# Kernel optimization log

Measured on AMD Instinct MI355X. Metric: run time of the kernel, lower is better.

Reference implementation:

```python
import jax, jax.numpy as jnp
import numpy as np

B = 4096      # number of trees
DEPTH = 7     # complete binary tree depth -> N = 2**DEPTH - 1 = 127 nodes (heap order)
I_DIM = 300
H_DIM = 150


def setup_inputs() -> dict:
    key = jax.random.key(0)
    ks = jax.random.split(key, 6)
    N = 2 ** DEPTH - 1
    x = jax.random.normal(ks[0], (B, N, I_DIM), dtype=jnp.float32)
    Wiuo = jax.random.normal(ks[1], (3 * H_DIM, I_DIM), dtype=jnp.float32) / np.sqrt(I_DIM)
    Uiuo = jax.random.normal(ks[2], (3 * H_DIM, H_DIM), dtype=jnp.float32) / np.sqrt(H_DIM)
    biuo = jax.random.normal(ks[3], (1, 3 * H_DIM), dtype=jnp.float32) * 0.02
    Uf_w = jax.random.normal(ks[4], (H_DIM, H_DIM), dtype=jnp.float32) / np.sqrt(H_DIM)
    Uf_b = jax.random.normal(ks[5], (H_DIM,), dtype=jnp.float32) * 0.02
    return {"x": x, "Wiuo": Wiuo, "Uiuo": Uiuo, "biuo": biuo, "Uf_w": Uf_w, "Uf_b": Uf_b}


def reference(x, Wiuo, Uiuo, biuo, Uf_w, Uf_b):
    # Child-sum Tree-LSTM on complete binary trees (heap ordering).
    # Level d occupies node indices [2^d - 1, 2^(d+1) - 1); leaves at d = DEPTH-1.
    Bsz, N, _ = x.shape
    H = Uf_w.shape[0]
    # Input projection for all nodes (dropout in eval mode = identity)
    iuo_x = jnp.einsum('bni,ki->bnk', x, Wiuo)  # [B, N, 3H]
    h = jnp.zeros((Bsz, N, H), x.dtype)
    c = jnp.zeros((Bsz, N, H), x.dtype)
    for d in reversed(range(DEPTH)):  # leaves -> root (static loop over tree levels)
        start = 2 ** d - 1
        size = 2 ** d
        iuo = iuo_x[:, start:start + size]  # [B, size, 3H]
        if d == DEPTH - 1:
            c_sum = jnp.zeros((Bsz, size, H), x.dtype)
        else:
            cstart = 2 ** (d + 1) - 1
            ch = h[:, cstart:cstart + 2 * size].reshape(Bsz, size, 2, H)
            cc = c[:, cstart:cstart + 2 * size].reshape(Bsz, size, 2, H)
            h_tilda = ch.sum(axis=2)  # sum of children hidden states
            f = jax.nn.sigmoid(jnp.einsum('bskh,gh->bskg', ch, Uf_w) + Uf_b)
            c_sum = (f * cc).sum(axis=2)
            iuo = iuo + jnp.einsum('bsh,kh->bsk', h_tilda, Uiuo)
        iuo = iuo + biuo
        i_g, u_g, o_g = jnp.split(iuo, 3, axis=-1)
        c_new = jax.nn.sigmoid(i_g) * jnp.tanh(u_g) + c_sum
        h_new = jax.nn.sigmoid(o_g) * jnp.tanh(c_new)
        h = h.at[:, start:start + size].set(h_new)
        c = c.at[:, start:start + size].set(c_new)
    return h
```

## Files before the change

kernel.cpp:

```cpp
#include <hip/hip_runtime.h>

typedef float  f32x4  __attribute__((ext_vector_type(4)));
typedef short  s16x8  __attribute__((ext_vector_type(8)));
typedef short  s16x4  __attribute__((ext_vector_type(4)));
typedef __bf16 bf16x8 __attribute__((ext_vector_type(8)));

namespace {
constexpr int BATCH = 4096, DEPTH_ = 7, NN = 127, CN = 126, IDIM = 300, HD = 150;
constexpr int NW = 10, NT = 640;
constexpr int XSTR = 328;
constexpr int CSTR = 164;
constexpr int BCS  = 40;

constexpr int WSLAB = 19456;
constexpr int FSLAB = 6656;
constexpr int WCH = 38, FCH = 13;
constexpr int W_SH = 10 * WSLAB, U_SH = 5 * WSLAB, F_SH = 5 * FSLAB;
constexpr size_t C_FLOATS = (size_t)BATCH * CN * HD;

constexpr int LEAF_XS = 128 * XSTR;
constexpr int INT_CHS = 128 * CSTR;
constexpr int INT_XS  = 64 * XSTR;
constexpr int LDS_LEAF_B = (LEAF_XS + 2 * WSLAB) * 2;
constexpr int LDS_INT_B  = (INT_CHS + INT_XS + 2 * WSLAB) * 2;

__device__ __forceinline__ short f2bf(float f) {
    union { __bf16 b; short s; } u; u.b = (__bf16)f; return u.s;
}
__device__ __forceinline__ float bf2f(short s) {
    union { float f; unsigned u; } v; v.u = ((unsigned)(unsigned short)s) << 16; return v.f;
}
__device__ __forceinline__ float sig_(float x)  { return 1.0f / (1.0f + __expf(-x)); }
__device__ __forceinline__ float tanh_(float x) { float e = __expf(2.0f * x); return 1.0f - 2.0f / (e + 1.0f); }

__device__ __forceinline__ f32x4 MFMA(s16x8 a, s16x8 b, f32x4 c) {
    return __builtin_amdgcn_mfma_f32_16x16x32_bf16(a, b, c, 0, 0, 0);
}

typedef const __attribute__((address_space(1))) unsigned int* gp_t;
typedef __attribute__((address_space(3))) unsigned int* lp_t;
__device__ __forceinline__ void stage_slab(const short* g, short* l, int nch, int wv, int ln) {
    const char* gb = (const char*)g;
    char* lb = (char*)l;
    for (int c = wv; c < nch; c += NW)
        __builtin_amdgcn_global_load_lds((gp_t)(gb + c * 1024 + ln * 16),
                                         (lp_t)(lb + c * 1024 + ln * 16), 16, 0, 0);
}
}

__global__ __launch_bounds__(256)
void prep_w(const float* __restrict__ Wiuo, const float* __restrict__ Uiuo,
            const float* __restrict__ Ufw, short* __restrict__ dst) {
    int i = blockIdx.x * 256 + threadIdx.x;
    short v = 0;
    if (i < W_SH) {
        int kb = i / WSLAB, r = i - kb * WSLAB;
        if (r < 480 * BCS) {
            int cs = r / BCS, j = r - cs * BCS;
            int g = cs / 160, cp = cs - g * 160, k = kb * 32 + j;
            if (cp < HD && j < 32 && k < IDIM) v = f2bf(Wiuo[(size_t)(g*HD + cp)*IDIM + k]);
        }
        dst[i] = v;
    } else if (i < W_SH + U_SH) {
        int q = i - W_SH;
        int kb = q / WSLAB, r = q - kb * WSLAB;
        if (r < 480 * BCS) {
            int cs = r / BCS, j = r - cs * BCS;
            int g = cs / 160, cp = cs - g * 160, k = kb * 32 + j;
            if (cp < HD && j < 32 && k < HD) v = f2bf(Uiuo[(size_t)(g*HD + cp)*HD + k]);
        }
        dst[i] = v;
    } else if (i < W_SH + U_SH + F_SH) {
        int q = i - W_SH - U_SH;
        int kb = q / FSLAB, r = q - kb * FSLAB;
        if (r < 160 * BCS) {
            int cs = r / BCS, j = r - cs * BCS, k = kb * 32 + j;
            if (cs < HD && j < 32 && k < HD) v = f2bf(Ufw[(size_t)cs*HD + k]);
        }
        dst[i] = v;
    }
}

template<bool INTERNAL>
__global__ __launch_bounds__(NT)
void lvl_kernel(const float* __restrict__ x,
                const short* __restrict__ Wsl, const short* __restrict__ Usl,
                const short* __restrict__ Fsl,
                const float* __restrict__ biuo, const float* __restrict__ Ufb,
                float* __restrict__ h_all, float* __restrict__ c_all,
                int start, int lg, int cstart)
{
    constexpr int MT = INTERNAL ? 4 : 8;
    constexpr int BM = 16 * MT;
    extern __shared__ short smem[];
    short* chs = smem;
    short* xs  = INTERNAL ? (smem + INT_CHS) : smem;
    short* fg  = xs;
    short* B0  = INTERNAL ? (smem + INT_CHS + INT_XS) : (smem + LEAF_XS);
    short* B1  = B0 + WSLAB;

    const int t    = threadIdx.x;
    const int wv   = t >> 6;
    const int ln   = t & 63;
    const int l15  = ln & 15;
    const int kg   = ln >> 4;
    const int row0 = blockIdx.x * BM;
    const int size = 1 << lg;
    const int c16  = 16 * wv;

    stage_slab(Wsl, B0, WCH, wv, ln);
    {
        constexpr int NQ = XSTR / 4;
        for (int q = t; q < BM * NQ; q += NT) {
            int lr = q / NQ, i0 = (q - lr * NQ) * 4;
            int row = row0 + lr, b = row >> lg, s = row & (size - 1);
            s16x4 v = {0,0,0,0};
            if (i0 < IDIM) {
                const float4 f = *(const float4*)(x + ((size_t)b*NN + start + s)*IDIM + i0);
                v = s16x4{ f2bf(f.x), f2bf(f.y), f2bf(f.z), f2bf(f.w) };
            }
            *(s16x4*)&xs[lr * XSTR + i0] = v;
        }
    }
    if (INTERNAL) {
        constexpr int NQ = CSTR / 4;
        for (int q = t; q < 2 * BM * NQ; q += NT) {
            int cl = q / NQ, i0 = (q - cl * NQ) * 4;
            int lr = cl >> 1, cc = cl & 1;
            int row = row0 + lr, b = row >> lg, s = row & (size - 1);
            const float* hp = h_all + ((size_t)b*NN + cstart + 2*s + cc) * HD;
            s16x4 v = {0,0,0,0};
            if (i0 + 3 < HD) {
                float2 f0 = *(const float2*)(hp + i0);
                float2 f1 = *(const float2*)(hp + i0 + 2);
                v = s16x4{ f2bf(f0.x), f2bf(f0.y), f2bf(f1.x), f2bf(f1.y) };
            } else if (i0 < HD) {
                float2 f0 = *(const float2*)(hp + i0);
                v = s16x4{ f2bf(f0.x), f2bf(f0.y), 0, 0 };
            }
            *(s16x4*)&chs[cl * CSTR + i0] = v;
        }
    }
    __syncthreads();

    f32x4 acc[MT][3] = {};

    #pragma unroll
    for (int kb = 0; kb < 10; ++kb) {
        short* bcur = (kb & 1) ? B1 : B0;
        short* bnxt = (kb & 1) ? B0 : B1;
        if (kb < 9)            stage_slab(Wsl + (kb+1)*WSLAB, bnxt, WCH, wv, ln);
        else if (INTERNAL)     stage_slab(Usl, bnxt, WCH, wv, ln);
        s16x8 a[MT];
        #pragma unroll
        for (int mt = 0; mt < MT; ++mt)
            a[mt] = *(const s16x8*)&xs[(16*mt + l15) * XSTR + kb*32 + kg*8];
        #pragma unroll
        for (int g = 0; g < 3; ++g) {
            s16x8 bf = *(const s16x8*)&bcur[(g*160 + c16 + l15) * BCS + kg*8];
            #pragma unroll
            for (int mt = 0; mt < MT; ++mt)
                acc[mt][g] = MFMA(a[mt], bf, acc[mt][g]);
        }
        __syncthreads();
    }

    f32x4 facc[2*MT] = {};

    if (INTERNAL) {
        #pragma unroll
        for (int ku = 0; ku < 5; ++ku) {
            int s = 10 + ku;
            short* bcur = (s & 1) ? B1 : B0;
            short* bnxt = (s & 1) ? B0 : B1;
            if (ku < 4) stage_slab(Usl + (ku+1)*WSLAB, bnxt, WCH, wv, ln);
            else        stage_slab(Fsl, bnxt, FCH, wv, ln);
            int ka = ku*32 + kg*8;
            s16x8 hs[MT];
            #pragma unroll
            for (int mt = 0; mt < MT; ++mt) {
                int pr = 16*mt + l15;
                s16x8 h0 = *(const s16x8*)&chs[(2*pr    ) * CSTR + ka];
                s16x8 h1 = *(const s16x8*)&chs[(2*pr + 1) * CSTR + ka];
                union { bf16x8 b; s16x8 s; } u0, u1, uo;
                u0.s = h0; u1.s = h1;
                #pragma unroll
                for (int e = 0; e < 8; ++e)
                    uo.b[e] = (__bf16)((float)u0.b[e] + (float)u1.b[e]);
                hs[mt] = uo.s;
            }
            #pragma unroll
            for (int g = 0; g < 3; ++g) {
                s16x8 bf = *(const s16x8*)&bcur[(g*160 + c16 + l15) * BCS + kg*8];
                #pragma unroll
                for (int mt = 0; mt < MT; ++mt)
                    acc[mt][g] = MFMA(hs[mt], bf, acc[mt][g]);
            }
            __syncthreads();
        }

        #pragma unroll
        for (int kf = 0; kf < 5; ++kf) {
            int s = 15 + kf;
            short* bcur = (s & 1) ? B1 : B0;
            short* bnxt = (s & 1) ? B0 : B1;
            if (kf < 4) stage_slab(Fsl + (kf+1)*FSLAB, bnxt, FCH, wv, ln);
            int ka = kf*32 + kg*8;
            s16x8 bf = *(const s16x8*)&bcur[(c16 + l15) * BCS + kg*8];
            #pragma unroll
            for (int rt = 0; rt < 2*MT; ++rt) {
                s16x8 af = *(const s16x8*)&chs[(16*rt + l15) * CSTR + ka];
                facc[rt] = MFMA(af, bf, facc[rt]);
            }
            __syncthreads();
        }

        {
            int c = c16 + l15;
            if (c < HD) {
                float fb_ = Ufb[c];
                #pragma unroll
                for (int rt = 0; rt < 2*MT; ++rt)
                    #pragma unroll
                    for (int r = 0; r < 4; ++r) {
                        int crow = 16*rt + 4*kg + r;
                        fg[crow * CSTR + c] = f2bf(sig_(facc[rt][r] + fb_));
                    }
            }
        }
        __syncthreads();
    }

    {
        int c = c16 + l15;
        if (c < HD) {
            float bi = biuo[c], bu = biuo[HD + c], bo = biuo[2*HD + c];
            #pragma unroll
            for (int mt = 0; mt < MT; ++mt)
                #pragma unroll
                for (int r = 0; r < 4; ++r) {
                    int pl = 16*mt + 4*kg + r;
                    int row = row0 + pl, b = row >> lg, s = row & (size - 1);
                    float ig = acc[mt][0][r] + bi;
                    float ug = acc[mt][1][r] + bu;
                    float og = acc[mt][2][r] + bo;
                    float csum = 0.0f;
                    if (INTERNAL) {
                        int cl = 2 * pl;
                        float f0 = bf2f(fg[(cl    ) * CSTR + c]);
                        float f1 = bf2f(fg[(cl + 1) * CSTR + c]);
                        const float* cp = c_all + ((size_t)b*CN + cstart + 2*s - 1) * HD + c;
                        csum = f0 * cp[0] + f1 * cp[HD];
                    }
                    float cn = sig_(ig) * tanh_(ug) + csum;
                    float hn = sig_(og) * tanh_(cn);
                    h_all[((size_t)b*NN + start + s) * HD + c] = hn;
                    if (start > 0)
                        c_all[((size_t)b*CN + start + s - 1) * HD + c] = cn;
                }
        }
    }
}

extern "C" void kernel_launch(void* const* d_in, const int* in_sizes, int n_in,
                              void* d_out, int out_size, void* d_ws, size_t ws_size,
                              hipStream_t stream) {
    const float* x    = (const float*)d_in[0];
    const float* Wiuo = (const float*)d_in[1];
    const float* Uiuo = (const float*)d_in[2];
    const float* biuo = (const float*)d_in[3];
    const float* Ufw  = (const float*)d_in[4];
    const float* Ufb  = (const float*)d_in[5];
    float* h = (float*)d_out;
    float* c = (float*)d_ws;
    short* wsl = (short*)((float*)d_ws + C_FLOATS);
    const short* Wsl = wsl;
    const short* Usl = wsl + W_SH;
    const short* Fsl = wsl + W_SH + U_SH;

    (void)hipFuncSetAttribute((const void*)lvl_kernel<false>,
                              hipFuncAttributeMaxDynamicSharedMemorySize, 160 * 1024);
    (void)hipFuncSetAttribute((const void*)lvl_kernel<true>,
                              hipFuncAttributeMaxDynamicSharedMemorySize, 160 * 1024);

    prep_w<<<(W_SH + U_SH + F_SH + 255) / 256, 256, 0, stream>>>(Wiuo, Uiuo, Ufw, wsl);

    for (int d = DEPTH_ - 1; d >= 0; --d) {
        const int size   = 1 << d;
        const int start  = size - 1;
        const int cstart = 2 * size - 1;
        if (d == DEPTH_ - 1) {
            const int blocks = (BATCH * size) / 128;
            lvl_kernel<false><<<blocks, NT, LDS_LEAF_B, stream>>>(
                x, Wsl, Usl, Fsl, biuo, Ufb, h, c, start, d, cstart);
        } else {
            const int blocks = (BATCH * size) / 64;
            lvl_kernel<true><<<blocks, NT, LDS_INT_B, stream>>>(
                x, Wsl, Usl, Fsl, biuo, Ufb, h, c, start, d, cstart);
        }
    }
}
```

Before: 1.279 ms.

## Split level kernel into input-GEMM and light recurrent kernels with fp16 intermediates

Splits each internal level into two kernels. A heavy x-projection GEMM writes fp16 iuo pre-activations to a slot buffer, and a light kernel computes the forget-gate and Uiuo products using 16-row blocks with weights read straight from global memory. Cell states move to ping-pong fp16 buffers, and the heavy kernel uses a single weight slab with occupancy bound 5 instead of double buffering. The aim is higher occupancy and less LDS pressure, paid for with extra launches, an extra global round-trip for iuo, reduced precision on stored c, and more syncs in the heavy kernel.

```diff
diff --git a/kernel.cpp b/kernel.cpp
--- a/kernel.cpp
+++ b/kernel.cpp
@@ -3,26 +3,26 @@
 typedef float  f32x4  __attribute__((ext_vector_type(4)));
 typedef short  s16x8  __attribute__((ext_vector_type(8)));
 typedef short  s16x4  __attribute__((ext_vector_type(4)));
-typedef __bf16 bf16x8 __attribute__((ext_vector_type(8)));
+typedef _Float16 f16;
 
 namespace {
-constexpr int BATCH = 4096, DEPTH_ = 7, NN = 127, CN = 126, IDIM = 300, HD = 150;
-constexpr int NW = 10, NT = 640;
-constexpr int XSTR = 328;
+constexpr int BATCH = 4096, NN = 127, IDIM = 300, HD = 150;
+constexpr int NT = 640, NW = 10;
+constexpr int XSTR = 324;
+constexpr int BCS  = 36;
+constexpr int WSLAB = 17408;
+constexpr int WCH = 34;
 constexpr int CSTR = 164;
-constexpr int BCS  = 40;
-
-constexpr int WSLAB = 19456;
-constexpr int FSLAB = 6656;
-constexpr int WCH = 38, FCH = 13;
-constexpr int W_SH = 10 * WSLAB, U_SH = 5 * WSLAB, F_SH = 5 * FSLAB;
-constexpr size_t C_FLOATS = (size_t)BATCH * CN * HD;
-
-constexpr int LEAF_XS = 128 * XSTR;
-constexpr int INT_CHS = 128 * CSTR;
-constexpr int INT_XS  = 64 * XSTR;
-constexpr int LDS_LEAF_B = (LEAF_XS + 2 * WSLAB) * 2;
-constexpr int LDS_INT_B  = (INT_CHS + INT_XS + 2 * WSLAB) * 2;
+
+constexpr size_t CA_N   = (size_t)BATCH * 64 * HD;
+constexpr size_t CB_N   = (size_t)BATCH * 32 * HD;
+constexpr size_t IUOA_N = (size_t)BATCH * 32 * 456;
+constexpr size_t IUOB_N = (size_t)BATCH * 16 * 456;
+constexpr int W_SH = 10 * WSLAB;
+constexpr int U_SH = 480 * 160;
+constexpr int F_SH = 160 * 160;
+
+constexpr int HEAVY_LDS = (64 * XSTR + WSLAB) * 2;
 
 __device__ __forceinline__ short f2bf(float f) {
     union { __bf16 b; short s; } u; u.b = (__bf16)f; return u.s;
@@ -32,7 +32,12 @@
 }
 __device__ __forceinline__ float sig_(float x)  { return 1.0f / (1.0f + __expf(-x)); }
 __device__ __forceinline__ float tanh_(float x) { float e = __expf(2.0f * x); return 1.0f - 2.0f / (e + 1.0f); }
-
+__device__ __forceinline__ s16x4 cvt4(float a,float b,float c,float d) {
+    return s16x4{ f2bf(a), f2bf(b), f2bf(c), f2bf(d) };
+}
+__device__ __forceinline__ s16x8 cat(s16x4 lo, s16x4 hi) {
+    return __builtin_shufflevector(lo, hi, 0,1,2,3,4,5,6,7);
+}
 __device__ __forceinline__ f32x4 MFMA(s16x8 a, s16x8 b, f32x4 c) {
     return __builtin_amdgcn_mfma_f32_16x16x32_bf16(a, b, c, 0, 0, 0);
 }
@@ -54,210 +59,224 @@
     int i = blockIdx.x * 256 + threadIdx.x;
     short v = 0;
     if (i < W_SH) {
-        int kb = i / WSLAB, r = i - kb * WSLAB;
+        int kc = i / WSLAB, r = i - kc * WSLAB;
         if (r < 480 * BCS) {
-            int cs = r / BCS, j = r - cs * BCS;
-            int g = cs / 160, cp = cs - g * 160, k = kb * 32 + j;
+            int col = r / BCS, j = r - col * BCS;
+            int g = col / 160, cp = col - g * 160, k = kc * 32 + j;
             if (cp < HD && j < 32 && k < IDIM) v = f2bf(Wiuo[(size_t)(g*HD + cp)*IDIM + k]);
         }
         dst[i] = v;
     } else if (i < W_SH + U_SH) {
         int q = i - W_SH;
-        int kb = q / WSLAB, r = q - kb * WSLAB;
-        if (r < 480 * BCS) {
-            int cs = r / BCS, j = r - cs * BCS;
-            int g = cs / 160, cp = cs - g * 160, k = kb * 32 + j;
-            if (cp < HD && j < 32 && k < HD) v = f2bf(Uiuo[(size_t)(g*HD + cp)*HD + k]);
-        }
+        int col = q / 160, k = q - col * 160;
+        int g = col / 160 >= 3 ? 2 : col / 160;
+        g = col / 160; int cp = col - g * 160;
+        if (cp < HD && k < HD) v = f2bf(Uiuo[(size_t)(g*HD + cp)*HD + k]);
         dst[i] = v;
     } else if (i < W_SH + U_SH + F_SH) {
         int q = i - W_SH - U_SH;
-        int kb = q / FSLAB, r = q - kb * FSLAB;
-        if (r < 160 * BCS) {
-            int cs = r / BCS, j = r - cs * BCS, k = kb * 32 + j;
-            if (cs < HD && j < 32 && k < HD) v = f2bf(Ufw[(size_t)cs*HD + k]);
-        }
+        int col = q / 160, k = q - col * 160;
+        if (col < HD && k < HD) v = f2bf(Ufw[(size_t)col*HD + k]);
         dst[i] = v;
     }
 }
 
-template<bool INTERNAL>
-__global__ __launch_bounds__(NT)
-void lvl_kernel(const float* __restrict__ x,
-                const short* __restrict__ Wsl, const short* __restrict__ Usl,
-                const short* __restrict__ Fsl,
-                const float* __restrict__ biuo, const float* __restrict__ Ufb,
-                float* __restrict__ h_all, float* __restrict__ c_all,
-                int start, int lg, int cstart)
+template<bool LEAF>
+__global__ __launch_bounds__(NT, 5)
+void gemm_x(const float* __restrict__ x, const short* __restrict__ Wsl,
+            const float* __restrict__ biuo, float* __restrict__ h_all,
+            f16* __restrict__ c_slot, f16* __restrict__ iuo_slot,
+            int start, int lg)
 {
-    constexpr int MT = INTERNAL ? 4 : 8;
-    constexpr int BM = 16 * MT;
     extern __shared__ short smem[];
-    short* chs = smem;
-    short* xs  = INTERNAL ? (smem + INT_CHS) : smem;
-    short* fg  = xs;
-    short* B0  = INTERNAL ? (smem + INT_CHS + INT_XS) : (smem + LEAF_XS);
-    short* B1  = B0 + WSLAB;
-
-    const int t    = threadIdx.x;
-    const int wv   = t >> 6;
-    const int ln   = t & 63;
-    const int l15  = ln & 15;
-    const int kg   = ln >> 4;
-    const int row0 = blockIdx.x * BM;
-    const int size = 1 << lg;
-    const int c16  = 16 * wv;
-
-    stage_slab(Wsl, B0, WCH, wv, ln);
+    short* xs  = smem;
+    short* wsl = smem + 64 * XSTR;
+
+    const int t   = threadIdx.x;
+    const int wv  = t >> 6, ln = t & 63, l15 = ln & 15, kg = ln >> 4;
+    const int row0 = blockIdx.x * 64;
+    const int mask = (1 << lg) - 1;
+    const int c16 = wv * 16;
+
+    stage_slab(Wsl, wsl, WCH, wv, ln);
     {
-        constexpr int NQ = XSTR / 4;
-        for (int q = t; q < BM * NQ; q += NT) {
-            int lr = q / NQ, i0 = (q - lr * NQ) * 4;
-            int row = row0 + lr, b = row >> lg, s = row & (size - 1);
-            s16x4 v = {0,0,0,0};
-            if (i0 < IDIM) {
-                const float4 f = *(const float4*)(x + ((size_t)b*NN + start + s)*IDIM + i0);
-                v = s16x4{ f2bf(f.x), f2bf(f.y), f2bf(f.z), f2bf(f.w) };
+        int lr = t & 63, seg = wv;
+        int row = row0 + lr, b = row >> lg, s = row & mask;
+        const float* xp = x + ((size_t)b*NN + start + s) * IDIM;
+        short* dst = &xs[lr * XSTR];
+        if (seg < 9) {
+            int e0 = seg * 32;
+            #pragma unroll
+            for (int q = 0; q < 8; ++q) {
+                float4 f = *(const float4*)(xp + e0 + 4*q);
+                *(s16x4*)&dst[e0 + 4*q] = cvt4(f.x, f.y, f.z, f.w);
             }
-            *(s16x4*)&xs[lr * XSTR + i0] = v;
-        }
-    }
-    if (INTERNAL) {
-        constexpr int NQ = CSTR / 4;
-        for (int q = t; q < 2 * BM * NQ; q += NT) {
-            int cl = q / NQ, i0 = (q - cl * NQ) * 4;
-            int lr = cl >> 1, cc = cl & 1;
-            int row = row0 + lr, b = row >> lg, s = row & (size - 1);
-            const float* hp = h_all + ((size_t)b*NN + cstart + 2*s + cc) * HD;
-            s16x4 v = {0,0,0,0};
-            if (i0 + 3 < HD) {
-                float2 f0 = *(const float2*)(hp + i0);
-                float2 f1 = *(const float2*)(hp + i0 + 2);
-                v = s16x4{ f2bf(f0.x), f2bf(f0.y), f2bf(f1.x), f2bf(f1.y) };
-            } else if (i0 < HD) {
-                float2 f0 = *(const float2*)(hp + i0);
-                v = s16x4{ f2bf(f0.x), f2bf(f0.y), 0, 0 };
+        } else {
+            #pragma unroll
+            for (int q = 0; q < 3; ++q) {
+                float4 f = *(const float4*)(xp + 288 + 4*q);
+                *(s16x4*)&dst[288 + 4*q] = cvt4(f.x, f.y, f.z, f.w);
             }
-            *(s16x4*)&chs[cl * CSTR + i0] = v;
+            #pragma unroll
+            for (int q = 0; q < 6; ++q) *(s16x4*)&dst[300 + 4*q] = s16x4{0,0,0,0};
         }
     }
     __syncthreads();
 
-    f32x4 acc[MT][3] = {};
-
+    f32x4 acc[4][3] = {};
     #pragma unroll
-    for (int kb = 0; kb < 10; ++kb) {
-        short* bcur = (kb & 1) ? B1 : B0;
-        short* bnxt = (kb & 1) ? B0 : B1;
-        if (kb < 9)            stage_slab(Wsl + (kb+1)*WSLAB, bnxt, WCH, wv, ln);
-        else if (INTERNAL)     stage_slab(Usl, bnxt, WCH, wv, ln);
-        s16x8 a[MT];
-        #pragma unroll
-        for (int mt = 0; mt < MT; ++mt)
-            a[mt] = *(const s16x8*)&xs[(16*mt + l15) * XSTR + kb*32 + kg*8];
+    for (int kc = 0; kc < 10; ++kc) {
+        int ka = kc * 32 + kg * 8;
+        s16x8 a[4];
+        #pragma unroll
+        for (int mt = 0; mt < 4; ++mt) {
+            const short* p = &xs[(16*mt + l15) * XSTR + ka];
+            a[mt] = cat(*(const s16x4*)p, *(const s16x4*)(p + 4));
+        }
         #pragma unroll
         for (int g = 0; g < 3; ++g) {
-            s16x8 bf = *(const s16x8*)&bcur[(g*160 + c16 + l15) * BCS + kg*8];
-            #pragma unroll
-            for (int mt = 0; mt < MT; ++mt)
+            const short* p = &wsl[(g*160 + c16 + l15) * BCS + kg * 8];
+            s16x8 bf = cat(*(const s16x4*)p, *(const s16x4*)(p + 4));
+            #pragma unroll
+            for (int mt = 0; mt < 4; ++mt)
                 acc[mt][g] = MFMA(a[mt], bf, acc[mt][g]);
         }
-        __syncthreads();
-    }
-
-    f32x4 facc[2*MT] = {};
-
-    if (INTERNAL) {
-        #pragma unroll
-        for (int ku = 0; ku < 5; ++ku) {
-            int s = 10 + ku;
-            short* bcur = (s & 1) ? B1 : B0;
-            short* bnxt = (s & 1) ? B0 : B1;
-            if (ku < 4) stage_slab(Usl + (ku+1)*WSLAB, bnxt, WCH, wv, ln);
-            else        stage_slab(Fsl, bnxt, FCH, wv, ln);
-            int ka = ku*32 + kg*8;
-            s16x8 hs[MT];
-            #pragma unroll
-            for (int mt = 0; mt < MT; ++mt) {
-                int pr = 16*mt + l15;
-                s16x8 h0 = *(const s16x8*)&chs[(2*pr    ) * CSTR + ka];
-                s16x8 h1 = *(const s16x8*)&chs[(2*pr + 1) * CSTR + ka];
-                union { bf16x8 b; s16x8 s; } u0, u1, uo;
-                u0.s = h0; u1.s = h1;
-                #pragma unroll
-                for (int e = 0; e < 8; ++e)
-                    uo.b[e] = (__bf16)((float)u0.b[e] + (float)u1.b[e]);
-                hs[mt] = uo.s;
-            }
-            #pragma unroll
-            for (int g = 0; g < 3; ++g) {
-                s16x8 bf = *(const s16x8*)&bcur[(g*160 + c16 + l15) * BCS + kg*8];
-                #pragma unroll
-                for (int mt = 0; mt < MT; ++mt)
-                    acc[mt][g] = MFMA(hs[mt], bf, acc[mt][g]);
-            }
+        if (kc < 9) {
             __syncthreads();
-        }
-
-        #pragma unroll
-        for (int kf = 0; kf < 5; ++kf) {
-            int s = 15 + kf;
-            short* bcur = (s & 1) ? B1 : B0;
-            short* bnxt = (s & 1) ? B0 : B1;
-            if (kf < 4) stage_slab(Fsl + (kf+1)*FSLAB, bnxt, FCH, wv, ln);
-            int ka = kf*32 + kg*8;
-            s16x8 bf = *(const s16x8*)&bcur[(c16 + l15) * BCS + kg*8];
-            #pragma unroll
-            for (int rt = 0; rt < 2*MT; ++rt) {
-                s16x8 af = *(const s16x8*)&chs[(16*rt + l15) * CSTR + ka];
-                facc[rt] = MFMA(af, bf, facc[rt]);
-            }
+            stage_slab(Wsl + (kc+1) * WSLAB, wsl, WCH, wv, ln);
             __syncthreads();
         }
-
-        {
-            int c = c16 + l15;
-            if (c < HD) {
-                float fb_ = Ufb[c];
-                #pragma unroll
-                for (int rt = 0; rt < 2*MT; ++rt)
-                    #pragma unroll
-                    for (int r = 0; r < 4; ++r) {
-                        int crow = 16*rt + 4*kg + r;
-                        fg[crow * CSTR + c] = f2bf(sig_(facc[rt][r] + fb_));
-                    }
-            }
-        }
-        __syncthreads();
-    }
-
-    {
-        int c = c16 + l15;
-        if (c < HD) {
+    }
+
+    int c = c16 + l15;
+    if (c < HD) {
+        if (LEAF) {
             float bi = biuo[c], bu = biuo[HD + c], bo = biuo[2*HD + c];
             #pragma unroll
-            for (int mt = 0; mt < MT; ++mt)
+            for (int mt = 0; mt < 4; ++mt)
                 #pragma unroll
                 for (int r = 0; r < 4; ++r) {
                     int pl = 16*mt + 4*kg + r;
-                    int row = row0 + pl, b = row >> lg, s = row & (size - 1);
-                    float ig = acc[mt][0][r] + bi;
-                    float ug = acc[mt][1][r] + bu;
-                    float og = acc[mt][2][r] + bo;
-                    float csum = 0.0f;
-                    if (INTERNAL) {
-                        int cl = 2 * pl;
-                        float f0 = bf2f(fg[(cl    ) * CSTR + c]);
-                        float f1 = bf2f(fg[(cl + 1) * CSTR + c]);
-                        const float* cp = c_all + ((size_t)b*CN + cstart + 2*s - 1) * HD + c;
-                        csum = f0 * cp[0] + f1 * cp[HD];
-                    }
-                    float cn = sig_(ig) * tanh_(ug) + csum;
-                    float hn = sig_(og) * tanh_(cn);
-                    h_all[((size_t)b*NN + start + s) * HD + c] = hn;
-                    if (start > 0)
-                        c_all[((size_t)b*CN + start + s - 1) * HD + c] = cn;
+                    int row = row0 + pl, b = row >> 6, n = row & 63;
+                    float cn = sig_(acc[mt][0][r] + bi) * tanh_(acc[mt][1][r] + bu);
+                    float hn = sig_(acc[mt][2][r] + bo) * tanh_(cn);
+                    h_all[((size_t)b*NN + 63 + n) * HD + c] = hn;
+                    c_slot[((size_t)(b*64 + n)) * HD + c] = (f16)cn;
                 }
+        } else {
+            #pragma unroll
+            for (int mt = 0; mt < 4; ++mt)
+                #pragma unroll
+                for (int r = 0; r < 4; ++r) {
+                    int row = row0 + 16*mt + 4*kg + r;
+                    f16* ip = iuo_slot + (size_t)row * 456;
+                    ip[c]        = (f16)acc[mt][0][r];
+                    ip[152 + c]  = (f16)acc[mt][1][r];
+                    ip[304 + c]  = (f16)acc[mt][2][r];
+                }
+        }
+    }
+}
+
+__global__ __launch_bounds__(NT, 5)
+void lvl_light(const short* __restrict__ Ubf, const short* __restrict__ Fbf,
+               const float* __restrict__ biuo, const float* __restrict__ Ufb,
+               const f16* __restrict__ iuo_slot, const f16* __restrict__ cprev,
+               f16* __restrict__ cmine, float* __restrict__ h_all,
+               int start, int lg, int cstart)
+{
+    __shared__ short chs[2][16][CSTR];
+    __shared__ short fgs[NW][32][16];
+
+    const int t = threadIdx.x;
+    const int wv = t >> 6, ln = t & 63, l15 = ln & 15, kg = ln >> 4;
+    const int row0 = blockIdx.x * 16;
+    const int mask = (1 << lg) - 1;
+    const int c = wv * 16 + l15;
+
+    {
+        int rc = t & 31, part = t >> 5;
+        int plane = rc >> 4, lr = rc & 15;
+        int row = row0 + lr, b = row >> lg, s = row & mask;
+        const float* hp = h_all + ((size_t)b*NN + cstart + 2*s + plane) * HD;
+        short* dst = &chs[plane][lr][part * 8];
+        if (part < 18) {
+            float4 f0 = *(const float4*)(hp + part*8);
+            float4 f1 = *(const float4*)(hp + part*8 + 4);
+            *(s16x4*)dst       = cvt4(f0.x, f0.y, f0.z, f0.w);
+            *(s16x4*)(dst + 4) = cvt4(f1.x, f1.y, f1.z, f1.w);
+        } else if (part == 18) {
+            float4 f0 = *(const float4*)(hp + 144);
+            float2 f1 = *(const float2*)(hp + 148);
+            *(s16x4*)dst       = cvt4(f0.x, f0.y, f0.z, f0.w);
+            *(s16x4*)(dst + 4) = s16x4{ f2bf(f1.x), f2bf(f1.y), 0, 0 };
+        } else {
+            *(s16x4*)dst = s16x4{0,0,0,0};
+            *(s16x4*)(dst + 4) = s16x4{0,0,0,0};
+        }
+    }
+    __syncthreads();
+
+    f32x4 facc[2] = {};
+    #pragma unroll
+    for (int kc = 0; kc < 5; ++kc) {
+        int ka = kc * 32 + kg * 8;
+        s16x8 bf = *(const s16x8*)(Fbf + (size_t)c * 160 + ka);
+        #pragma unroll
+        for (int rt = 0; rt < 2; ++rt) {
+            const short* p = &chs[rt][l15][ka];
+            s16x8 af = cat(*(const s16x4*)p, *(const s16x4*)(p + 4));
+            facc[rt] = MFMA(af, bf, facc[rt]);
+        }
+    }
+    {
+        float fb_ = (c < HD) ? Ufb[c] : 0.0f;
+        #pragma unroll
+        for (int rt = 0; rt < 2; ++rt)
+            #pragma unroll
+            for (int r = 0; r < 4; ++r)
+                fgs[wv][rt*16 + 4*kg + r][l15] = f2bf(sig_(facc[rt][r] + fb_));
+    }
+    __syncthreads();
+
+    f32x4 acc[3] = {};
+    #pragma unroll
+    for (int kc = 0; kc < 5; ++kc) {
+        int ka = kc * 32 + kg * 8;
+        const short* p0 = &chs[0][l15][ka];
+        const short* p1 = &chs[1][l15][ka];
+        s16x8 h0 = cat(*(const s16x4*)p0, *(const s16x4*)(p0 + 4));
+        s16x8 h1 = cat(*(const s16x4*)p1, *(const s16x4*)(p1 + 4));
+        s16x8 hs;
+        #pragma unroll
+        for (int e = 0; e < 8; ++e)
+            hs[e] = f2bf(bf2f(h0[e]) + bf2f(h1[e]));
+        #pragma unroll
+        for (int g = 0; g < 3; ++g) {
+            s16x8 bf = *(const s16x8*)(Ubf + (size_t)(g*160 + c) * 160 + ka);
+            acc[g] = MFMA(hs, bf, acc[g]);
+        }
+    }
+
+    if (c < HD) {
+        float bi = biuo[c], bu = biuo[HD + c], bo = biuo[2*HD + c];
+        #pragma unroll
+        for (int r = 0; r < 4; ++r) {
+            int pl = 4*kg + r;
+            int row = row0 + pl, b = row >> lg, s = row & mask;
+            const f16* ip = iuo_slot + (size_t)row * 456;
+            float ig = (float)ip[c]       + bi + acc[0][r];
+            float ug = (float)ip[152 + c] + bu + acc[1][r];
+            float og = (float)ip[304 + c] + bo + acc[2][r];
+            float f0 = bf2f(fgs[wv][pl][l15]);
+            float f1 = bf2f(fgs[wv][16 + pl][l15]);
+            size_t cb = ((size_t)b << (lg + 1)) + 2*s;
+            float c0 = (float)cprev[(cb    ) * HD + c];
+            float c1 = (float)cprev[(cb + 1) * HD + c];
+            float cn = sig_(ig) * tanh_(ug) + f0*c0 + f1*c1;
+            float hn = sig_(og) * tanh_(cn);
+            h_all[((size_t)b*NN + start + s) * HD + c] = hn;
+            cmine[(((size_t)b << lg) + s) * HD + c] = (f16)cn;
         }
     }
 }
@@ -272,31 +291,32 @@
     const float* Ufw  = (const float*)d_in[4];
     const float* Ufb  = (const float*)d_in[5];
     float* h = (float*)d_out;
-    float* c = (float*)d_ws;
-    short* wsl = (short*)((float*)d_ws + C_FLOATS);
-    const short* Wsl = wsl;
-    const short* Usl = wsl + W_SH;
-    const short* Fsl = wsl + W_SH + U_SH;
-
-    (void)hipFuncSetAttribute((const void*)lvl_kernel<false>,
+
+    f16* cA   = (f16*)d_ws;
+    f16* cB   = cA + CA_N;
+    f16* iuoA = cB + CB_N;
+    f16* iuoB = iuoA + IUOA_N;
+    short* slabs = (short*)(iuoB + IUOB_N);
+    const short* Wsl = slabs;
+    const short* Ubf = slabs + W_SH;
+    const short* Fbf = slabs + W_SH + U_SH;
+
+    (void)hipFuncSetAttribute((const void*)gemm_x<true>,
                               hipFuncAttributeMaxDynamicSharedMemorySize, 160 * 1024);
-    (void)hipFuncSetAttribute((const void*)lvl_kernel<true>,
+    (void)hipFuncSetAttribute((const void*)gemm_x<false>,
                               hipFuncAttributeMaxDynamicSharedMemorySize, 160 * 1024);
 
-    prep_w<<<(W_SH + U_SH + F_SH + 255) / 256, 256, 0, stream>>>(Wiuo, Uiuo, Ufw, wsl);
-
-    for (int d = DEPTH_ - 1; d >= 0; --d) {
-        const int size   = 1 << d;
-        const int start  = size - 1;
-        const int cstart = 2 * size - 1;
-        if (d == DEPTH_ - 1) {
-            const int blocks = (BATCH * size) / 128;
-            lvl_kernel<false><<<blocks, NT, LDS_LEAF_B, stream>>>(
-                x, Wsl, Usl, Fsl, biuo, Ufb, h, c, start, d, cstart);
-        } else {
-            const int blocks = (BATCH * size) / 64;
-            lvl_kernel<true><<<blocks, NT, LDS_INT_B, stream>>>(
-                x, Wsl, Usl, Fsl, biuo, Ufb, h, c, start, d, cstart);
-        }
-    }
-}
+    prep_w<<<(W_SH + U_SH + F_SH + 255) / 256, 256, 0, stream>>>(Wiuo, Uiuo, Ufw, slabs);
+
+    gemm_x<true><<<4096, NT, HEAVY_LDS, stream>>>(x, Wsl, biuo, h, cA, nullptr, 63, 6);
+
+    for (int d = 5; d >= 0; --d) {
+        f16* islot = (d & 1) ? iuoA : iuoB;
+        f16* cprev = ((d + 1) & 1) ? cB : cA;
+        f16* cmine = (d & 1) ? cB : cA;
+        const int start = (1 << d) - 1, cstart = (1 << (d+1)) - 1;
+        gemm_x<false><<<64 << d, NT, HEAVY_LDS, stream>>>(x, Wsl, biuo, h, nullptr, islot, start, d);
+        lvl_light<<<256 << d, NT, 0, stream>>>(Ubf, Fbf, biuo, Ufb, islot, cprev, cmine, h,
+                                               start, d, cstart);
+    }
+}
```

Result: faster. 1.104 ms (-13.7%).
